# Kernel tuning notes

Measured on AMD Instinct MI355X. Metric: run time of the kernel, lower is better.

The kernel has to match this reference:

```python
import jax, jax.numpy as jnp
import numpy as np

STEPS = 200
H = 0.5
N_POP = 100000.0
CLAMP = 100000.0
BATCH = 65536


def setup_inputs() -> dict:
    key = jax.random.key(0)
    k1, k2 = jax.random.split(key)
    # init state [B, 1, 4] = (S, E, I, R); positive values
    init = jax.random.uniform(k1, (BATCH, 1, 4), dtype=jnp.float32) * 1000.0
    # weights mirrors nn.Parameter([100000, 3, 6, 0, 0.5, 0.2, 0.25]) with small noise
    base = jnp.array([100000.0, 3.0, 6.0, 0.0, 0.5, 0.2, 0.25], dtype=jnp.float32)
    weights = base + 0.01 * jax.random.normal(k2, (7,), dtype=jnp.float32)
    return {"init": init, "weights": weights}


def reference(init, weights):
    A, B, C = weights[4], weights[5], weights[6]

    def step(x, _):
        # x: [B, 1, 4]
        s, e, i = x[:, 0, 0], x[:, 0, 1], x[:, 0, 2]
        infl = B * s * (e + i) / N_POP
        d = jnp.stack((-infl, infl - A * e, A * e - C * i, C * i), axis=-1)  # [B, 4]
        x_new = x + H * jnp.clip(d[:, None, :], -CLAMP, CLAMP)  # [B, 1, 4]
        return x_new, x_new

    _, outs = jax.lax.scan(step, init, None, length=STEPS)  # [steps, B, 1, 4]
    return jnp.moveaxis(outs, 0, 1)  # [B, steps, 1, 4]
```

## Files before the change

kernel.cpp:

```cpp
#include <hip/hip_runtime.h>

#define BATCH   65536
#define STEPS   200
#define TCHUNK  8
#define NCHUNK  (STEPS / TCHUNK)
#define BLK     64
#define LSTRIDE 33

__global__ __launch_bounds__(BLK) void seir_kernel(
    const float* __restrict__ init,
    const float* __restrict__ w,
    float* __restrict__ out)
{
    __shared__ float lds[BLK * LSTRIDE];

    const int lane   = threadIdx.x;
    const int base_b = blockIdx.x * BLK;
    const int b      = base_b + lane;

    const float A = w[4];
    const float B = w[5];
    const float C = w[6];
    const float invN = 1.0f / 100000.0f;

    float4 x = reinterpret_cast<const float4*>(init)[b];
    float4* outf4 = reinterpret_cast<float4*>(out);

    for (int chunk = 0; chunk < NCHUNK; ++chunk) {
        #pragma unroll
        for (int tt = 0; tt < TCHUNK; ++tt) {
            float infl = B * x.x * (x.y + x.z) * invN;
            float ae = A * x.y;
            float ci = C * x.z;
            float d0 = -infl;
            float d1 = infl - ae;
            float d2 = ae - ci;
            float d3 = ci;
            d0 = fminf(fmaxf(d0, -100000.0f), 100000.0f);
            d1 = fminf(fmaxf(d1, -100000.0f), 100000.0f);
            d2 = fminf(fmaxf(d2, -100000.0f), 100000.0f);
            d3 = fminf(fmaxf(d3, -100000.0f), 100000.0f);
            x.x += 0.5f * d0;
            x.y += 0.5f * d1;
            x.z += 0.5f * d2;
            x.w += 0.5f * d3;
            const int a = lane * LSTRIDE + tt * 4;
            lds[a + 0] = x.x;
            lds[a + 1] = x.y;
            lds[a + 2] = x.z;
            lds[a + 3] = x.w;
        }
        __syncthreads();

        const int t0 = chunk * TCHUNK;
        #pragma unroll
        for (int k = 0; k < 8; ++k) {
            const int s  = k * BLK + lane;
            const int bb = s >> 3;
            const int j  = s & 7;
            const int a  = bb * LSTRIDE + j * 4;
            float4 v = make_float4(lds[a + 0], lds[a + 1], lds[a + 2], lds[a + 3]);
            outf4[(size_t)(base_b + bb) * STEPS + t0 + j] = v;
        }
        __syncthreads();
    }
}

extern "C" void kernel_launch(void* const* d_in, const int* in_sizes, int n_in,
                              void* d_out, int out_size, void* d_ws, size_t ws_size,
                              hipStream_t stream) {
    const float* init = (const float*)d_in[0];
    const float* w    = (const float*)d_in[1];
    float* out        = (float*)d_out;

    seir_kernel<<<dim3(BATCH / BLK), dim3(BLK), 0, stream>>>(init, w, out);
}
```

Measured before the change: 204.0 us.

## Double-buffer LDS staging, drop barriers, and vectorize LDS accesses

Stages simulation steps into two alternating LDS buffers, so the global stores of one chunk can overlap the compute of the next. Both __syncthreads calls are removed, relying on the 64-thread block being a single wavefront. LDS reads and writes become float4 accesses, with the row stride padded to 36 for 16-byte alignment. The risk is that correctness now depends on wave64 lockstep and on the compiler keeping cross-lane LDS stores and loads in order without a barrier; the padding may also change the LDS bank-conflict pattern.

After: 203.9 us. Within noise of the previous version (-0.1%).

```diff
diff --git a/kernel.cpp b/kernel.cpp
--- a/kernel.cpp
+++ b/kernel.cpp
@@ -5,18 +5,70 @@
 #define TCHUNK  8
 #define NCHUNK  (STEPS / TCHUNK)
 #define BLK     64
-#define LSTRIDE 33
+#define LSTRIDE 36
+
+__device__ __forceinline__ void step_and_stash(
+    float4& x, float A, float B, float C, float invN,
+    float* __restrict__ buf, int lane, int tt)
+{
+    float infl = B * x.x * (x.y + x.z) * invN;
+    float ae = A * x.y;
+    float ci = C * x.z;
+    float d0 = -infl;
+    float d1 = infl - ae;
+    float d2 = ae - ci;
+    float d3 = ci;
+    d0 = fminf(fmaxf(d0, -100000.0f), 100000.0f);
+    d1 = fminf(fmaxf(d1, -100000.0f), 100000.0f);
+    d2 = fminf(fmaxf(d2, -100000.0f), 100000.0f);
+    d3 = fminf(fmaxf(d3, -100000.0f), 100000.0f);
+    x.x += 0.5f * d0;
+    x.y += 0.5f * d1;
+    x.z += 0.5f * d2;
+    x.w += 0.5f * d3;
+    *reinterpret_cast<float4*>(&buf[lane * LSTRIDE + tt * 4]) = x;
+}
+
+__device__ __forceinline__ void compute_chunk(
+    float4& x, float A, float B, float C, float invN,
+    float* __restrict__ buf, int lane)
+{
+    #pragma unroll
+    for (int tt = 0; tt < TCHUNK; ++tt)
+        step_and_stash(x, A, B, C, invN, buf, lane, tt);
+}
+
+__device__ __forceinline__ void flush_chunk(
+    const float* __restrict__ buf, float4* __restrict__ outf4,
+    int base_b, int bbase, int jj, int t0)
+{
+    float4 f[8];
+    #pragma unroll
+    for (int k = 0; k < 8; ++k) {
+        const int bb = k * 8 + bbase;
+        f[k] = *reinterpret_cast<const float4*>(&buf[bb * LSTRIDE + jj * 4]);
+    }
+    #pragma unroll
+    for (int k = 0; k < 8; ++k) {
+        const int bb = k * 8 + bbase;
+        outf4[(size_t)(base_b + bb) * STEPS + t0 + jj] = f[k];
+    }
+}
 
 __global__ __launch_bounds__(BLK) void seir_kernel(
     const float* __restrict__ init,
     const float* __restrict__ w,
     float* __restrict__ out)
 {
-    __shared__ float lds[BLK * LSTRIDE];
+    __shared__ float ldsA[BLK * LSTRIDE];
+    __shared__ float ldsB[BLK * LSTRIDE];
 
     const int lane   = threadIdx.x;
     const int base_b = blockIdx.x * BLK;
     const int b      = base_b + lane;
+
+    const int jj    = lane & 7;
+    const int bbase = lane >> 3;
 
     const float A = w[4];
     const float B = w[5];
@@ -26,44 +78,15 @@
     float4 x = reinterpret_cast<const float4*>(init)[b];
     float4* outf4 = reinterpret_cast<float4*>(out);
 
-    for (int chunk = 0; chunk < NCHUNK; ++chunk) {
-        #pragma unroll
-        for (int tt = 0; tt < TCHUNK; ++tt) {
-            float infl = B * x.x * (x.y + x.z) * invN;
-            float ae = A * x.y;
-            float ci = C * x.z;
-            float d0 = -infl;
-            float d1 = infl - ae;
-            float d2 = ae - ci;
-            float d3 = ci;
-            d0 = fminf(fmaxf(d0, -100000.0f), 100000.0f);
-            d1 = fminf(fmaxf(d1, -100000.0f), 100000.0f);
-            d2 = fminf(fmaxf(d2, -100000.0f), 100000.0f);
-            d3 = fminf(fmaxf(d3, -100000.0f), 100000.0f);
-            x.x += 0.5f * d0;
-            x.y += 0.5f * d1;
-            x.z += 0.5f * d2;
-            x.w += 0.5f * d3;
-            const int a = lane * LSTRIDE + tt * 4;
-            lds[a + 0] = x.x;
-            lds[a + 1] = x.y;
-            lds[a + 2] = x.z;
-            lds[a + 3] = x.w;
-        }
-        __syncthreads();
+    compute_chunk(x, A, B, C, invN, ldsA, lane);
 
-        const int t0 = chunk * TCHUNK;
-        #pragma unroll
-        for (int k = 0; k < 8; ++k) {
-            const int s  = k * BLK + lane;
-            const int bb = s >> 3;
-            const int j  = s & 7;
-            const int a  = bb * LSTRIDE + j * 4;
-            float4 v = make_float4(lds[a + 0], lds[a + 1], lds[a + 2], lds[a + 3]);
-            outf4[(size_t)(base_b + bb) * STEPS + t0 + j] = v;
-        }
-        __syncthreads();
+    for (int c = 1; c < NCHUNK; c += 2) {
+        flush_chunk(ldsA, outf4, base_b, bbase, jj, (c - 1) * TCHUNK);
+        compute_chunk(x, A, B, C, invN, ldsB, lane);
+        flush_chunk(ldsB, outf4, base_b, bbase, jj, c * TCHUNK);
+        compute_chunk(x, A, B, C, invN, ldsA, lane);
     }
+    flush_chunk(ldsA, outf4, base_b, bbase, jj, (NCHUNK - 1) * TCHUNK);
 }
 
 extern "C" void kernel_launch(void* const* d_in, const int* in_sizes, int n_in,
```
